# Kernel tuning notes

Hardware: AMD Instinct MI355X
Metric: run time of the kernel (lower is better)

Reference implementation:

```python
import jax, jax.numpy as jnp
import numpy as np

NUM_EXPERTS = 8
HIDDEN = 1024
INTER = 2048
TOKENS = 2048
TOP_K = 2


def setup_inputs() -> dict:
    key = jax.random.key(0)
    k1, k2, k3, k4, k5 = jax.random.split(key, 5)
    hidden_states = jax.random.normal(k1, (TOKENS, HIDDEN), dtype=jnp.float32)
    top_k_index = jax.random.randint(k2, (TOKENS, TOP_K), 0, NUM_EXPERTS, dtype=jnp.int64)
    top_k_weights = jax.random.uniform(k3, (TOKENS, TOP_K), dtype=jnp.float32)
    # parameters, scaled like typical init
    gate_up_proj = jax.random.normal(k4, (NUM_EXPERTS, 2 * INTER, HIDDEN), dtype=jnp.float32) * (HIDDEN ** -0.5)
    down_proj = jax.random.normal(k5, (NUM_EXPERTS, HIDDEN, INTER), dtype=jnp.float32) * (INTER ** -0.5)
    return {
        "hidden_states": hidden_states,
        "top_k_index": top_k_index,
        "top_k_weights": top_k_weights,
        "gate_up_proj": gate_up_proj,
        "down_proj": down_proj,
    }


def reference(hidden_states, top_k_index, top_k_weights, gate_up_proj, down_proj):
    # combine weights per (token, expert): w[t, e] = sum_k 1[idx[t,k]==e] * tw[t,k]
    one_hot = jax.nn.one_hot(top_k_index, NUM_EXPERTS, dtype=hidden_states.dtype)  # [T, K, E]
    combine = jnp.einsum("tke,tk->te", one_hot, top_k_weights)  # [T, E]

    out = jnp.zeros_like(hidden_states)
    # fixed small loop over experts (structural, not a data dim)
    for e in range(NUM_EXPERTS):
        gu = hidden_states @ gate_up_proj[e].T  # [T, 2I]
        gate, up = jnp.split(gu, 2, axis=-1)
        h = jax.nn.gelu(gate, approximate=True) * up  # gelu_pytorch_tanh
        y = h @ down_proj[e].T  # [T, H]
        out = out + y * combine[:, e][:, None]
    return out
```

## Files before the change

### kernel.cpp

```cpp
#include <hip/hip_runtime.h>
#include <stdint.h>

#define T_TOK  2048
#define HID    1024
#define INTERN 2048
#define NEXP   8
#define MAXPOS 5248

typedef __attribute__((ext_vector_type(8))) short          bf16x8;
typedef __attribute__((ext_vector_type(4))) float          f32x4;
typedef __attribute__((ext_vector_type(8))) unsigned short u16x8;
typedef __attribute__((ext_vector_type(4))) unsigned short u16x4;

__device__ __forceinline__ unsigned short f32_to_bf16(float f) {
  unsigned int u = __float_as_uint(f);
  unsigned int r = (u + 0x7FFFu + ((u >> 16) & 1u)) >> 16;
  return (unsigned short)r;
}

__device__ __forceinline__ float bf16_to_f32(unsigned short h) {
  unsigned int u = ((unsigned int)h) << 16;
  return __uint_as_float(u);
}

__device__ __forceinline__ void gload_lds16(const void* g, void* l) {
  __builtin_amdgcn_global_load_lds(
      (const __attribute__((address_space(1))) unsigned int*)g,
      (__attribute__((address_space(3))) unsigned int*)l, 16, 0, 0);
}

__device__ __forceinline__ u16x8 cvt8(float4 a, float4 b) {
  u16x8 w;
  w[0] = f32_to_bf16(a.x); w[1] = f32_to_bf16(a.y);
  w[2] = f32_to_bf16(a.z); w[3] = f32_to_bf16(a.w);
  w[4] = f32_to_bf16(b.x); w[5] = f32_to_bf16(b.y);
  w[6] = f32_to_bf16(b.z); w[7] = f32_to_bf16(b.w);
  return w;
}

#define WAIT_VM0()    asm volatile("s_waitcnt vmcnt(0)" ::: "memory")
#define WAIT_LGKM0()  asm volatile("s_waitcnt lgkmcnt(0)" ::: "memory")
#define SCHED_FENCE() __builtin_amdgcn_sched_barrier(0)

__global__ void route_kernel(const int* __restrict__ tki,
                             const float* __restrict__ tkw,
                             int* __restrict__ counts,
                             int* __restrict__ offsets,
                             int* __restrict__ tok_list,
                             float* __restrict__ w_list,
                             int* __restrict__ pos_map,
                             float* __restrict__ wgt_map) {
  __shared__ int scnt[NEXP];
  __shared__ int soff[NEXP];
  int tid = threadIdx.x;
  if (tid < NEXP) scnt[tid] = 0;
  __syncthreads();
  for (int t = tid; t < T_TOK; t += 256) {
    int e0 = tki[2 * t] & 7;
    int e1 = tki[2 * t + 1] & 7;
    float w0 = tkw[2 * t];
    float w1 = tkw[2 * t + 1];
    if (e0 == e1) {
      int p = atomicAdd(&scnt[e0], 1);
      tok_list[e0 * T_TOK + p] = t;
      w_list [e0 * T_TOK + p] = w0 + w1;
      pos_map[2 * t]     = (p << 3) | e0;
      wgt_map[2 * t]     = w0 + w1;
      pos_map[2 * t + 1] = -1;
      wgt_map[2 * t + 1] = 0.0f;
    } else {
      int p = atomicAdd(&scnt[e0], 1);
      tok_list[e0 * T_TOK + p] = t;
      w_list [e0 * T_TOK + p] = w0;
      pos_map[2 * t]     = (p << 3) | e0;
      wgt_map[2 * t]     = w0;
      int q = atomicAdd(&scnt[e1], 1);
      tok_list[e1 * T_TOK + q] = t;
      w_list [e1 * T_TOK + q] = w1;
      pos_map[2 * t + 1] = (q << 3) | e1;
      wgt_map[2 * t + 1] = w1;
    }
  }
  __syncthreads();
  if (tid == 0) {
    int acc = 0;
    for (int e = 0; e < NEXP; ++e) {
      counts[e]  = scnt[e];
      offsets[e] = acc;
      soff[e]    = acc;
      acc += ((scnt[e] + 127) >> 7) << 7;
    }
  }
  __syncthreads();
  for (int i = tid; i < 2 * T_TOK; i += 256) {
    int v = pos_map[i];
    if (v >= 0) pos_map[i] = soff[v & 7] + (v >> 3);
  }
}

__global__ void cvt_x_kernel(const float* __restrict__ x, unsigned short* __restrict__ xb) {
  int i = blockIdx.x * 256 + threadIdx.x;
  float4 v = ((const float4*)x)[i];
  u16x4 o;
  o[0] = f32_to_bf16(v.x); o[1] = f32_to_bf16(v.y);
  o[2] = f32_to_bf16(v.z); o[3] = f32_to_bf16(v.w);
  *((u16x4*)(xb + 4 * (size_t)i)) = o;
}

__global__ void gather_x_kernel(const unsigned short* __restrict__ xb,
                                const int* __restrict__ counts,
                                const int* __restrict__ offsets,
                                const int* __restrict__ tok_list,
                                unsigned short* __restrict__ xg) {
  int p = blockIdx.x * 128 + threadIdx.x;
  int c = blockIdx.y;
  int e = 0;
#pragma unroll
  for (int k = 1; k < NEXP; ++k) if (p >= offsets[k]) e = k;
  int r = p - offsets[e];
  u16x8 v = (u16x8){0, 0, 0, 0, 0, 0, 0, 0};
  if (r < counts[e]) {
    int tok = tok_list[e * T_TOK + r];
    v = *((const u16x8*)(xb + (size_t)tok * HID + c * 8));
  }
  *((u16x8*)(xg + (size_t)(p >> 7) * 131072 + c * 1024 + (p & 127) * 8)) = v;
}

__global__ __launch_bounds__(256, 4)
void gemm1_kernel(const unsigned short* __restrict__ xg,
                  const float* __restrict__ gup,
                  const int* __restrict__ counts,
                  const int* __restrict__ offsets,
                  unsigned short* __restrict__ hbuf) {
  int e  = blockIdx.z;
  int Ne = counts[e];
  int m0 = blockIdx.y * 128;
  if (m0 >= Ne) return;
  int n0  = blockIdx.x * 64;
  int off = offsets[e];

  __shared__ __align__(16) unsigned short As[2][4][128][8];
  __shared__ __align__(16) unsigned short Gs[2][4][64][8];
  __shared__ __align__(16) unsigned short Us[2][4][64][8];

  int tid  = threadIdx.x;
  int lane = tid & 63;
  int wave = tid >> 6;
  int wm = wave >> 1;
  int wn = wave & 1;

  const unsigned short* asrc = xg + (size_t)((off + m0) >> 7) * (HID * 128);

  int brow = tid >> 2;
  int bq   = tid & 3;
  const float* gsrc = gup + (size_t)e * (2 * INTERN) * HID + (size_t)(n0 + brow) * HID + bq * 8;
  const float* usrc = gsrc + (size_t)INTERN * HID;
  int brw = brow ^ bq;

  f32x4 accg[4][2], accu[4][2];
#pragma unroll
  for (int m = 0; m < 4; ++m)
#pragma unroll
    for (int n = 0; n < 2; ++n) {
      accg[m][n] = (f32x4){0.f, 0.f, 0.f, 0.f};
      accu[m][n] = (f32x4){0.f, 0.f, 0.f, 0.f};
    }

  float4 g0, g1, u0, u1;

  {
    const float4* gp = (const float4*)gsrc;
    const float4* up = (const float4*)usrc;
    g0 = gp[0]; g1 = gp[1];
    u0 = up[0]; u1 = up[1];
    char* base = (char*)&As[0][0][0][0];
    gload_lds16(asrc + (size_t)tid * 8,        base + (size_t)tid * 16);
    gload_lds16(asrc + 2048 + (size_t)tid * 8, base + 4096 + (size_t)tid * 16);
    *((u16x8*)&Gs[0][bq][brw][0]) = cvt8(g0, g1);
    *((u16x8*)&Us[0][bq][brw][0]) = cvt8(u0, u1);
    WAIT_LGKM0(); SCHED_FENCE();
  }

  int cur = 0;
  const int NT = HID / 32;
  for (int t = 0; t < NT; ++t) {
    WAIT_VM0(); SCHED_FENCE();
    __builtin_amdgcn_s_barrier(); SCHED_FENCE();
    int nxt = cur ^ 1;
    int kn = (t + 1 < NT) ? (t + 1) * 32 : 0;
    {
      const float4* gp = (const float4*)(gsrc + kn);
      const float4* up = (const float4*)(usrc + kn);
      g0 = gp[0]; g1 = gp[1];
      u0 = up[0]; u1 = up[1];
    }
    {
      char* base = (char*)&As[nxt][0][0][0];
      const unsigned short* ak = asrc + (size_t)kn * 128;
      gload_lds16(ak + (size_t)tid * 8,        base + (size_t)tid * 16);
      gload_lds16(ak + 2048 + (size_t)tid * 8, base + 4096 + (size_t)tid * 16);
    }
    SCHED_FENCE();
    {
      int kg = lane >> 4;
      int rl = lane & 15;
      bf16x8 af[4], gf[2], uf[2];
#pragma unroll
      for (int m = 0; m < 4; ++m)
        af[m] = *((const bf16x8*)&As[cur][kg][wm * 64 + m * 16 + rl][0]);
#pragma unroll
      for (int n = 0; n < 2; ++n) {
        int r = (wn * 32 + n * 16 + rl) ^ kg;
        gf[n] = *((const bf16x8*)&Gs[cur][kg][r][0]);
        uf[n] = *((const bf16x8*)&Us[cur][kg][r][0]);
      }
#pragma unroll
      for (int m = 0; m < 4; ++m)
#pragma unroll
        for (int n = 0; n < 2; ++n) {
          accg[m][n] = __builtin_amdgcn_mfma_f32_16x16x32_bf16(af[m], gf[n], accg[m][n], 0, 0, 0);
          accu[m][n] = __builtin_amdgcn_mfma_f32_16x16x32_bf16(af[m], uf[n], accu[m][n], 0, 0, 0);
        }
    }
    *((u16x8*)&Gs[nxt][bq][brw][0]) = cvt8(g0, g1);
    *((u16x8*)&Us[nxt][bq][brw][0]) = cvt8(u0, u1);
    WAIT_LGKM0(); SCHED_FENCE();
    cur = nxt;
  }
  WAIT_VM0();

  int rl = lane & 15;
  int rq = lane >> 4;
  size_t hb_base = (size_t)((off + m0) >> 7) * (INTERN * 128);
#pragma unroll
  for (int m = 0; m < 4; ++m) {
#pragma unroll
    for (int n = 0; n < 2; ++n) {
      int col = n0 + wn * 32 + n * 16 + rl;
      size_t cbase = hb_base + (size_t)(col >> 3) * 1024 + (col & 7);
#pragma unroll
      for (int j = 0; j < 4; ++j) {
        int lr = wm * 64 + m * 16 + rq * 4 + j;
        if (m0 + lr < Ne) {
          float gv = accg[m][n][j];
          float uv = accu[m][n][j];
          float tt2 = gv + 0.044715f * gv * gv * gv;
          float a  = gv / (1.0f + __expf(-1.5957691216f * tt2));
          hbuf[cbase + (size_t)lr * 8] = f32_to_bf16(a * uv);
        }
      }
    }
  }
}

__global__ __launch_bounds__(256, 2)
void gemm2_kernel(const unsigned short* __restrict__ hbuf,
                  const float* __restrict__ down,
                  const int* __restrict__ counts,
                  const int* __restrict__ offsets,
                  unsigned short* __restrict__ ybuf) {
  int e  = blockIdx.z;
  int Ne = counts[e];
  int m0 = blockIdx.y * 128;
  if (m0 >= Ne) return;
  int n0  = blockIdx.x * 64;
  int off = offsets[e];

  __shared__ __align__(16) unsigned short As[2][8][128][8];
  __shared__ __align__(16) unsigned short Bs[2][8][64][8];

  int tid  = threadIdx.x;
  int lane = tid & 63;
  int wave = tid >> 6;
  int wm = wave >> 1;
  int wn = wave & 1;

  const unsigned short* asrc = hbuf + (size_t)((off + m0) >> 7) * (INTERN * 128);

  int brow = tid >> 2;
  int bq   = tid & 3;
  int kgw0 = bq * 2, kgw1 = bq * 2 + 1;
  const float* bsrc = down + (size_t)e * HID * INTERN + (size_t)(n0 + brow) * INTERN + bq * 16;

  f32x4 acc[4][2];
#pragma unroll
  for (int m = 0; m < 4; ++m)
#pragma unroll
    for (int n = 0; n < 2; ++n) acc[m][n] = (f32x4){0.f, 0.f, 0.f, 0.f};

  float4 b0, b1, b2, b3;

  {
    const float4* bp = (const float4*)bsrc;
    b0 = bp[0]; b1 = bp[1]; b2 = bp[2]; b3 = bp[3];
    char* base = (char*)&As[0][0][0][0];
#pragma unroll
    for (int o = 0; o < 4; ++o)
      gload_lds16(asrc + o * 2048 + (size_t)tid * 8, base + o * 4096 + (size_t)tid * 16);
    *((u16x8*)&Bs[0][kgw0][brow ^ kgw0][0]) = cvt8(b0, b1);
    *((u16x8*)&Bs[0][kgw1][brow ^ kgw1][0]) = cvt8(b2, b3);
    WAIT_LGKM0(); SCHED_FENCE();
  }

  int cur = 0;
  const int NT = INTERN / 64;
  for (int t = 0; t < NT; ++t) {
    WAIT_VM0(); SCHED_FENCE();
    __builtin_amdgcn_s_barrier(); SCHED_FENCE();
    int nxt = cur ^ 1;
    int kn = (t + 1 < NT) ? (t + 1) * 64 : 0;
    {
      const float4* bp = (const float4*)(bsrc + kn);
      b0 = bp[0]; b1 = bp[1]; b2 = bp[2]; b3 = bp[3];
    }
    {
      char* base = (char*)&As[nxt][0][0][0];
      const unsigned short* ak = asrc + (size_t)kn * 128;
#pragma unroll
      for (int o = 0; o < 4; ++o)
        gload_lds16(ak + o * 2048 + (size_t)tid * 8, base + o * 4096 + (size_t)tid * 16);
    }
    SCHED_FENCE();
#pragma unroll
    for (int kk = 0; kk < 2; ++kk) {
      int kg = kk * 4 + (lane >> 4);
      int rl = lane & 15;
      bf16x8 af[4], bfv[2];
#pragma unroll
      for (int m = 0; m < 4; ++m)
        af[m] = *((const bf16x8*)&As[cur][kg][wm * 64 + m * 16 + rl][0]);
#pragma unroll
      for (int n = 0; n < 2; ++n)
        bfv[n] = *((const bf16x8*)&Bs[cur][kg][(wn * 32 + n * 16 + rl) ^ kg][0]);
#pragma unroll
      for (int m = 0; m < 4; ++m)
#pragma unroll
        for (int n = 0; n < 2; ++n)
          acc[m][n] = __builtin_amdgcn_mfma_f32_16x16x32_bf16(af[m], bfv[n], acc[m][n], 0, 0, 0);
    }
    *((u16x8*)&Bs[nxt][kgw0][brow ^ kgw0][0]) = cvt8(b0, b1);
    *((u16x8*)&Bs[nxt][kgw1][brow ^ kgw1][0]) = cvt8(b2, b3);
    WAIT_LGKM0(); SCHED_FENCE();
    cur = nxt;
  }
  WAIT_VM0();

  int rl = lane & 15;
  int rq = lane >> 4;
#pragma unroll
  for (int m = 0; m < 4; ++m) {
#pragma unroll
    for (int n = 0; n < 2; ++n) {
      int col = n0 + wn * 32 + n * 16 + rl;
#pragma unroll
      for (int j = 0; j < 4; ++j) {
        int lr = wm * 64 + m * 16 + rq * 4 + j;
        if (m0 + lr < Ne)
          ybuf[(size_t)(off + m0 + lr) * HID + col] = f32_to_bf16(acc[m][n][j]);
      }
    }
  }
}

__global__ void combine_kernel(const int* __restrict__ pos_map,
                               const float* __restrict__ wgt_map,
                               const unsigned short* __restrict__ ybuf,
                               float* __restrict__ out) {
  int i  = blockIdx.x * 256 + threadIdx.x;
  int t  = i >> 7;
  int c8 = i & 127;
  int p0 = pos_map[2 * t];
  int p1 = pos_map[2 * t + 1];
  float w0 = wgt_map[2 * t];
  float w1 = wgt_map[2 * t + 1];
  float acc[8];
#pragma unroll
  for (int j = 0; j < 8; ++j) acc[j] = 0.f;
  if (p0 >= 0) {
    u16x8 v = *((const u16x8*)(ybuf + (size_t)p0 * HID + c8 * 8));
#pragma unroll
    for (int j = 0; j < 8; ++j) acc[j] += w0 * bf16_to_f32(v[j]);
  }
  if (p1 >= 0) {
    u16x8 v = *((const u16x8*)(ybuf + (size_t)p1 * HID + c8 * 8));
#pragma unroll
    for (int j = 0; j < 8; ++j) acc[j] += w1 * bf16_to_f32(v[j]);
  }
  float4 o0 = make_float4(acc[0], acc[1], acc[2], acc[3]);
  float4 o1 = make_float4(acc[4], acc[5], acc[6], acc[7]);
  float4* dst = (float4*)(out + (size_t)t * HID + c8 * 8);
  dst[0] = o0;
  dst[1] = o1;
}

extern "C" void kernel_launch(void* const* d_in, const int* in_sizes, int n_in,
                              void* d_out, int out_size, void* d_ws, size_t ws_size,
                              hipStream_t stream) {
  (void)in_sizes; (void)n_in; (void)out_size;
  const float* hidden = (const float*)d_in[0];
  const int*   tki    = (const int*)d_in[1];
  const float* tkw    = (const float*)d_in[2];
  const float* gup    = (const float*)d_in[3];
  const float* down   = (const float*)d_in[4];
  float* out = (float*)d_out;
  char*  ws  = (char*)d_ws;

  int*   counts   = (int*)  (ws + 0);
  int*   offsets  = (int*)  (ws + 64);
  int*   tok_list = (int*)  (ws + 256);
  int*   pos_map  = (int*)  (ws + 65792);
  float* wgt_map  = (float*)(ws + 82176);
  float* w_list   = (float*)(ws + 98560);
  unsigned short* xb   = (unsigned short*)(ws + 164096);
  unsigned short* hbuf = (unsigned short*)(ws + 4358400);
  unsigned short* ybuf = (unsigned short*)(ws + 25854208);
  unsigned short* xg   = ybuf;

  if (ws_size < 36602112ull) return;

  hipLaunchKernelGGL(route_kernel, dim3(1), dim3(256), 0, stream,
                     tki, tkw, counts, offsets, tok_list, w_list, pos_map, wgt_map);
  hipLaunchKernelGGL(cvt_x_kernel, dim3((T_TOK * HID / 4) / 256), dim3(256), 0, stream,
                     hidden, xb);
  hipLaunchKernelGGL(gather_x_kernel, dim3(MAXPOS / 128, 128), dim3(128), 0, stream,
                     xb, counts, offsets, tok_list, xg);
  hipLaunchKernelGGL(gemm1_kernel, dim3(INTERN / 64, T_TOK / 128, NEXP), dim3(256), 0, stream,
                     xg, gup, counts, offsets, hbuf);
  hipLaunchKernelGGL(gemm2_kernel, dim3(HID / 64, T_TOK / 128, NEXP), dim3(256), 0, stream,
                     hbuf, down, counts, offsets, ybuf);
  hipLaunchKernelGGL(combine_kernel, dim3(T_TOK * HID / 8 / 256), dim3(256), 0, stream,
                     pos_map, wgt_map, ybuf, out);
}
```

Before: 148.5 us.

## Prefetch weight tiles two stages ahead, fuse gather with bf16 conversion, packed cvt

Both GEMM kernels now issue the fp32 weight loads two k-steps ahead and wait only until at most four vector loads are outstanding, so weight-load latency overlaps a full MFMA iteration instead of being drained each step. The separate fp32-to-bf16 conversion kernel and the gather kernel are merged into one launch that reads fp32 hidden rows directly and converts them while writing the grouped layout. The bf16 conversion uses the packed hardware instruction in place of the manual rounding code. The vmcnt(4) wait depends on exactly four register loads being issued after the LDS-direct loads, which is fragile if the compiler reorders them.

```diff
diff --git a/kernel.cpp b/kernel.cpp
--- a/kernel.cpp
+++ b/kernel.cpp
@@ -30,15 +30,16 @@
 }
 
 __device__ __forceinline__ u16x8 cvt8(float4 a, float4 b) {
-  u16x8 w;
-  w[0] = f32_to_bf16(a.x); w[1] = f32_to_bf16(a.y);
-  w[2] = f32_to_bf16(a.z); w[3] = f32_to_bf16(a.w);
-  w[4] = f32_to_bf16(b.x); w[5] = f32_to_bf16(b.y);
-  w[6] = f32_to_bf16(b.z); w[7] = f32_to_bf16(b.w);
-  return w;
+  union { u16x8 s; unsigned int u[4]; } r;
+  asm("v_cvt_pk_bf16_f32 %0, %1, %2" : "=v"(r.u[0]) : "v"(a.x), "v"(a.y));
+  asm("v_cvt_pk_bf16_f32 %0, %1, %2" : "=v"(r.u[1]) : "v"(a.z), "v"(a.w));
+  asm("v_cvt_pk_bf16_f32 %0, %1, %2" : "=v"(r.u[2]) : "v"(b.x), "v"(b.y));
+  asm("v_cvt_pk_bf16_f32 %0, %1, %2" : "=v"(r.u[3]) : "v"(b.z), "v"(b.w));
+  return r.s;
 }
 
 #define WAIT_VM0()    asm volatile("s_waitcnt vmcnt(0)" ::: "memory")
+#define WAIT_VM4()    asm volatile("s_waitcnt vmcnt(4)" ::: "memory")
 #define WAIT_LGKM0()  asm volatile("s_waitcnt lgkmcnt(0)" ::: "memory")
 #define SCHED_FENCE() __builtin_amdgcn_sched_barrier(0)
 
@@ -98,32 +99,24 @@
   }
 }
 
-__global__ void cvt_x_kernel(const float* __restrict__ x, unsigned short* __restrict__ xb) {
-  int i = blockIdx.x * 256 + threadIdx.x;
-  float4 v = ((const float4*)x)[i];
-  u16x4 o;
-  o[0] = f32_to_bf16(v.x); o[1] = f32_to_bf16(v.y);
-  o[2] = f32_to_bf16(v.z); o[3] = f32_to_bf16(v.w);
-  *((u16x4*)(xb + 4 * (size_t)i)) = o;
-}
-
-__global__ void gather_x_kernel(const unsigned short* __restrict__ xb,
-                                const int* __restrict__ counts,
-                                const int* __restrict__ offsets,
-                                const int* __restrict__ tok_list,
-                                unsigned short* __restrict__ xg) {
-  int p = blockIdx.x * 128 + threadIdx.x;
-  int c = blockIdx.y;
+__global__ void gather_cvt_x_kernel(const float* __restrict__ hidden,
+                                    const int* __restrict__ counts,
+                                    const int* __restrict__ offsets,
+                                    const int* __restrict__ tok_list,
+                                    unsigned short* __restrict__ xg) {
+  int p = blockIdx.x * 2 + (threadIdx.x >> 7);
+  int c = threadIdx.x & 127;
   int e = 0;
 #pragma unroll
   for (int k = 1; k < NEXP; ++k) if (p >= offsets[k]) e = k;
   int r = p - offsets[e];
-  u16x8 v = (u16x8){0, 0, 0, 0, 0, 0, 0, 0};
+  float4 a = {0.f, 0.f, 0.f, 0.f}, b = {0.f, 0.f, 0.f, 0.f};
   if (r < counts[e]) {
     int tok = tok_list[e * T_TOK + r];
-    v = *((const u16x8*)(xb + (size_t)tok * HID + c * 8));
-  }
-  *((u16x8*)(xg + (size_t)(p >> 7) * 131072 + c * 1024 + (p & 127) * 8)) = v;
+    const float4* src = (const float4*)(hidden + (size_t)tok * HID + c * 8);
+    a = src[0]; b = src[1];
+  }
+  *((u16x8*)(xg + (size_t)(p >> 7) * 131072 + c * 1024 + (p & 127) * 8)) = cvt8(a, b);
 }
 
 __global__ __launch_bounds__(256, 4)
@@ -169,34 +162,30 @@
   float4 g0, g1, u0, u1;
 
   {
-    const float4* gp = (const float4*)gsrc;
-    const float4* up = (const float4*)usrc;
-    g0 = gp[0]; g1 = gp[1];
-    u0 = up[0]; u1 = up[1];
     char* base = (char*)&As[0][0][0][0];
     gload_lds16(asrc + (size_t)tid * 8,        base + (size_t)tid * 16);
     gload_lds16(asrc + 2048 + (size_t)tid * 8, base + 4096 + (size_t)tid * 16);
-    *((u16x8*)&Gs[0][bq][brw][0]) = cvt8(g0, g1);
-    *((u16x8*)&Us[0][bq][brw][0]) = cvt8(u0, u1);
+    const float4* gp = (const float4*)gsrc;
+    const float4* up = (const float4*)usrc;
+    float4 tg0 = gp[0], tg1 = gp[1], tu0 = up[0], tu1 = up[1];
+    *((u16x8*)&Gs[0][bq][brw][0]) = cvt8(tg0, tg1);
+    *((u16x8*)&Us[0][bq][brw][0]) = cvt8(tu0, tu1);
+    const float4* gp1 = (const float4*)(gsrc + 32);
+    const float4* up1 = (const float4*)(usrc + 32);
+    g0 = gp1[0]; g1 = gp1[1]; u0 = up1[0]; u1 = up1[1];
     WAIT_LGKM0(); SCHED_FENCE();
   }
 
   int cur = 0;
   const int NT = HID / 32;
   for (int t = 0; t < NT; ++t) {
-    WAIT_VM0(); SCHED_FENCE();
+    WAIT_VM4(); SCHED_FENCE();
     __builtin_amdgcn_s_barrier(); SCHED_FENCE();
     int nxt = cur ^ 1;
-    int kn = (t + 1 < NT) ? (t + 1) * 32 : 0;
-    {
-      const float4* gp = (const float4*)(gsrc + kn);
-      const float4* up = (const float4*)(usrc + kn);
-      g0 = gp[0]; g1 = gp[1];
-      u0 = up[0]; u1 = up[1];
-    }
+    int ka = (t + 1 < NT) ? (t + 1) * 32 : 0;
     {
       char* base = (char*)&As[nxt][0][0][0];
-      const unsigned short* ak = asrc + (size_t)kn * 128;
+      const unsigned short* ak = asrc + (size_t)ka * 128;
       gload_lds16(ak + (size_t)tid * 8,        base + (size_t)tid * 16);
       gload_lds16(ak + 2048 + (size_t)tid * 8, base + 4096 + (size_t)tid * 16);
     }
@@ -224,6 +213,13 @@
     }
     *((u16x8*)&Gs[nxt][bq][brw][0]) = cvt8(g0, g1);
     *((u16x8*)&Us[nxt][bq][brw][0]) = cvt8(u0, u1);
+    SCHED_FENCE();
+    {
+      int kb = (t + 2 < NT) ? (t + 2) * 32 : 0;
+      const float4* gp = (const float4*)(gsrc + kb);
+      const float4* up = (const float4*)(usrc + kb);
+      g0 = gp[0]; g1 = gp[1]; u0 = up[0]; u1 = up[1];
+    }
     WAIT_LGKM0(); SCHED_FENCE();
     cur = nxt;
   }
@@ -291,31 +287,29 @@
   float4 b0, b1, b2, b3;
 
   {
-    const float4* bp = (const float4*)bsrc;
-    b0 = bp[0]; b1 = bp[1]; b2 = bp[2]; b3 = bp[3];
     char* base = (char*)&As[0][0][0][0];
 #pragma unroll
     for (int o = 0; o < 4; ++o)
       gload_lds16(asrc + o * 2048 + (size_t)tid * 8, base + o * 4096 + (size_t)tid * 16);
-    *((u16x8*)&Bs[0][kgw0][brow ^ kgw0][0]) = cvt8(b0, b1);
-    *((u16x8*)&Bs[0][kgw1][brow ^ kgw1][0]) = cvt8(b2, b3);
+    const float4* bp = (const float4*)bsrc;
+    float4 t0 = bp[0], t1 = bp[1], t2 = bp[2], t3 = bp[3];
+    *((u16x8*)&Bs[0][kgw0][brow ^ kgw0][0]) = cvt8(t0, t1);
+    *((u16x8*)&Bs[0][kgw1][brow ^ kgw1][0]) = cvt8(t2, t3);
+    const float4* bp1 = (const float4*)(bsrc + 64);
+    b0 = bp1[0]; b1 = bp1[1]; b2 = bp1[2]; b3 = bp1[3];
     WAIT_LGKM0(); SCHED_FENCE();
   }
 
   int cur = 0;
   const int NT = INTERN / 64;
   for (int t = 0; t < NT; ++t) {
-    WAIT_VM0(); SCHED_FENCE();
+    WAIT_VM4(); SCHED_FENCE();
     __builtin_amdgcn_s_barrier(); SCHED_FENCE();
     int nxt = cur ^ 1;
-    int kn = (t + 1 < NT) ? (t + 1) * 64 : 0;
-    {
-      const float4* bp = (const float4*)(bsrc + kn);
-      b0 = bp[0]; b1 = bp[1]; b2 = bp[2]; b3 = bp[3];
-    }
+    int ka = (t + 1 < NT) ? (t + 1) * 64 : 0;
     {
       char* base = (char*)&As[nxt][0][0][0];
-      const unsigned short* ak = asrc + (size_t)kn * 128;
+      const unsigned short* ak = asrc + (size_t)ka * 128;
 #pragma unroll
       for (int o = 0; o < 4; ++o)
         gload_lds16(ak + o * 2048 + (size_t)tid * 8, base + o * 4096 + (size_t)tid * 16);
@@ -340,6 +334,12 @@
     }
     *((u16x8*)&Bs[nxt][kgw0][brow ^ kgw0][0]) = cvt8(b0, b1);
     *((u16x8*)&Bs[nxt][kgw1][brow ^ kgw1][0]) = cvt8(b2, b3);
+    SCHED_FENCE();
+    {
+      int kb = (t + 2 < NT) ? (t + 2) * 64 : 0;
+      const float4* bp = (const float4*)(bsrc + kb);
+      b0 = bp[0]; b1 = bp[1]; b2 = bp[2]; b3 = bp[3];
+    }
     WAIT_LGKM0(); SCHED_FENCE();
     cur = nxt;
   }
@@ -411,7 +411,6 @@
   int*   pos_map  = (int*)  (ws + 65792);
   float* wgt_map  = (float*)(ws + 82176);
   float* w_list   = (float*)(ws + 98560);
-  unsigned short* xb   = (unsigned short*)(ws + 164096);
   unsigned short* hbuf = (unsigned short*)(ws + 4358400);
   unsigned short* ybuf = (unsigned short*)(ws + 25854208);
   unsigned short* xg   = ybuf;
@@ -420,10 +419,8 @@
 
   hipLaunchKernelGGL(route_kernel, dim3(1), dim3(256), 0, stream,
                      tki, tkw, counts, offsets, tok_list, w_list, pos_map, wgt_map);
-  hipLaunchKernelGGL(cvt_x_kernel, dim3((T_TOK * HID / 4) / 256), dim3(256), 0, stream,
-                     hidden, xb);
-  hipLaunchKernelGGL(gather_x_kernel, dim3(MAXPOS / 128, 128), dim3(128), 0, stream,
-                     xb, counts, offsets, tok_list, xg);
+  hipLaunchKernelGGL(gather_cvt_x_kernel, dim3(MAXPOS / 2), dim3(256), 0, stream,
+                     hidden, counts, offsets, tok_list, xg);
   hipLaunchKernelGGL(gemm1_kernel, dim3(INTERN / 64, T_TOK / 128, NEXP), dim3(256), 0, stream,
                      xg, gup, counts, offsets, hbuf);
   hipLaunchKernelGGL(gemm2_kernel, dim3(HID / 64, T_TOK / 128, NEXP), dim3(256), 0, stream,
```

New measurement: 139.3 us. -6.2%, faster.
